# Kernel tuning notes

Measured on AMD Instinct MI355X. Metric: run time of the kernel, lower is better.

## Reference

```python
import jax, jax.numpy as jnp
import numpy as np

H, D = 8, 32          # num_heads, head dim (hidden = 256)
HID = H * D
LRELU = 0.2
NT, NC, E, FIN = 60000, 30000, 200000, 64


def setup_inputs() -> dict:
    key = jax.random.key(0)
    ks = jax.random.split(key, 24)
    s = 0.05
    inp = {
        'x_trans': jax.random.normal(ks[0], (NT, FIN), jnp.float32),
        'x_cc':    jax.random.normal(ks[1], (NC, FIN), jnp.float32),
        'src_c2t': jax.random.randint(ks[2], (E,), 0, NC),
        'dst_c2t': jax.random.randint(ks[3], (E,), 0, NT),
        'src_t2c': jax.random.randint(ks[4], (E,), 0, NT),
        'dst_t2c': jax.random.randint(ks[5], (E,), 0, NC),
        'W_in': jax.random.normal(ks[6], (2, FIN, HID), jnp.float32) * s,
        'b_in': jnp.zeros((2, HID), jnp.float32),
        'Wk': jax.random.normal(ks[7], (2, 2, HID, HID), jnp.float32) * s,
        'bk': jnp.zeros((2, 2, HID), jnp.float32),
        'Wq': jax.random.normal(ks[8], (2, 2, HID, HID), jnp.float32) * s,
        'bq': jnp.zeros((2, 2, HID), jnp.float32),
        'Wv': jax.random.normal(ks[9], (2, 2, HID, HID), jnp.float32) * s,
        'bv': jnp.zeros((2, 2, HID), jnp.float32),
        'Wa': jax.random.normal(ks[10], (2, 2, HID, HID), jnp.float32) * s,
        'ba': jnp.zeros((2, 2, HID), jnp.float32),
        'a_rel': jax.random.normal(ks[11], (2, 2, H, D, D), jnp.float32) * s,
        'm_rel': jax.random.normal(ks[12], (2, 2, H, D, D), jnp.float32) * s,
        'p_rel': jnp.ones((2, 2, H), jnp.float32),
        'skip':  jnp.ones((2, 2), jnp.float32),
        'W_out': jax.random.normal(ks[13], (HID, 64), jnp.float32) * s,
        'b_out': jnp.zeros((64,), jnp.float32),
    }
    return inp


def _hgt_layer(xs, Wk, bk, Wq, bq, Wv, bv, Wa, ba, a_rel, m_rel, p_rel, skip, edges):
    # xs: list of [N_t, HID] per node type; edges: list of (src_type, dst_type, src_idx, dst_idx)
    nt = len(xs)
    k = [(xs[t] @ Wk[t] + bk[t]).reshape(-1, H, D) for t in range(nt)]
    q = [(xs[t] @ Wq[t] + bq[t]).reshape(-1, H, D) for t in range(nt)]
    v = [(xs[t] @ Wv[t] + bv[t]).reshape(-1, H, D) for t in range(nt)]
    agg = [jnp.zeros((xs[t].shape[0], H, D), xs[t].dtype) for t in range(nt)]
    inv_sqrt_d = 1.0 / jnp.sqrt(jnp.float32(D))
    for r, (st, dt, si, di) in enumerate(edges):
        kr = jnp.einsum('nhd,hde->nhe', k[st], a_rel[r])   # relation-transformed keys
        vr = jnp.einsum('nhd,hde->nhe', v[st], m_rel[r])   # relation-transformed messages
        ke, ve, qe = kr[si], vr[si], q[dt][di]             # [E, H, D] gathers
        alpha = jnp.einsum('ehd,ehd->eh', qe, ke) * p_rel[r] * inv_sqrt_d  # [E, H]
        n_dst = xs[dt].shape[0]
        m = jax.ops.segment_max(alpha, di, num_segments=n_dst)
        ex = jnp.exp(alpha - m[di])
        ssum = jax.ops.segment_sum(ex, di, num_segments=n_dst)
        w = ex / (ssum[di] + 1e-16)                         # segment softmax per dst node
        agg[dt] = agg[dt] + jax.ops.segment_sum(ve * w[..., None], di, num_segments=n_dst)
    out = []
    for t in range(nt):
        o = jax.nn.gelu(agg[t].reshape(-1, HID), approximate=False)
        o = o @ Wa[t] + ba[t]
        beta = jax.nn.sigmoid(skip[t])
        out.append(beta * o + (1.0 - beta) * xs[t])
    return out


def reference(x_trans, x_cc, src_c2t, dst_c2t, src_t2c, dst_t2c,
              W_in, b_in, Wk, bk, Wq, bq, Wv, bv, Wa, ba,
              a_rel, m_rel, p_rel, skip, W_out, b_out):
    # per-node-type Linear + in-place relu
    xs = [jax.nn.relu(x_trans @ W_in[0] + b_in[0]),
          jax.nn.relu(x_cc @ W_in[1] + b_in[1])]
    # relation 0: cc_node -> trans_node ; relation 1: trans_node -> cc_node
    edges = [(1, 0, src_c2t, dst_c2t), (0, 1, src_t2c, dst_t2c)]
    n_layers = Wk.shape[0]
    for l in range(n_layers):
        xs = _hgt_layer(xs, Wk[l], bk[l], Wq[l], bq[l], Wv[l], bv[l], Wa[l], ba[l],
                        a_rel[l], m_rel[l], p_rel[l], skip[l], edges)
    # dropout is identity in eval mode
    y = xs[0] @ W_out + b_out
    y = jnp.where(y > 0, y, LRELU * y)                      # LeakyReLU(0.2)
    n = jnp.linalg.norm(y, axis=1, keepdims=True)
    return y / jnp.maximum(n, 1e-12)                        # F.normalize(p=2, dim=1)
```

## Files before the change

kernel.cpp:

```cpp
#include <hip/hip_runtime.h>
#include <hip/hip_bf16.h>
#include <math.h>

#define NTN 60000
#define NCN 30000
#define NED 200000

typedef unsigned short u16;
typedef __attribute__((ext_vector_type(8))) u16 u16x8;
typedef __attribute__((ext_vector_type(8))) __bf16 bf16x8;
typedef __attribute__((ext_vector_type(4))) float f32x4;

static __device__ __forceinline__ float bf2f(u16 u) {
    return __uint_as_float(((unsigned)u) << 16);
}
static __device__ __forceinline__ u16 f2bf(float f) {
    unsigned u = __float_as_uint(f);
    unsigned r = (u + 0x7fffu + ((u >> 16) & 1u)) >> 16;
    return (u16)r;
}

__global__ void fill_u32(unsigned* __restrict__ p, unsigned v, int n) {
    int i = blockIdx.x * blockDim.x + threadIdx.x;
    int stride = gridDim.x * blockDim.x;
    for (; i < n; i += stride) p[i] = v;
}

__global__ void f32_to_bf16(const float* __restrict__ in, u16* __restrict__ out, int n4) {
    int i = blockIdx.x * blockDim.x + threadIdx.x;
    int stride = gridDim.x * blockDim.x;
    for (; i < n4; i += stride) {
        float4 v = ((const float4*)in)[i];
        ushort4 o;
        o.x = f2bf(v.x); o.y = f2bf(v.y); o.z = f2bf(v.z); o.w = f2bf(v.w);
        ((ushort4*)out)[i] = o;
    }
}

__global__ void convTb(const float* __restrict__ in, u16* __restrict__ out,
                       int K, int N, int inStride, int outStride, int nm) {
    int idx = blockIdx.x * blockDim.x + threadIdx.x;
    int per = N * (K >> 2);
    int total = per * nm;
    if (idx >= total) return;
    int mat = idx / per, rem = idx - mat * per;
    int k4 = rem / N, n = rem - k4 * N;
    int k = k4 * 4;
    const float* src = in + (size_t)mat * inStride;
    u16* dst = out + (size_t)mat * outStride;
    ushort4 o;
    o.x = f2bf(src[(size_t)(k + 0) * N + n]);
    o.y = f2bf(src[(size_t)(k + 1) * N + n]);
    o.z = f2bf(src[(size_t)(k + 2) * N + n]);
    o.w = f2bf(src[(size_t)(k + 3) * N + n]);
    *(ushort4*)(dst + (size_t)n * K + k) = o;
}

__global__ void copy_bq(const float* __restrict__ bq, float* __restrict__ bqkv) {
    int lt = blockIdx.x;
    bqkv[lt * 768 + threadIdx.x] = bq[lt * 256 + threadIdx.x];
}

__global__ __launch_bounds__(256) void fuse_weights(
    const float* __restrict__ Wk, const float* __restrict__ bk,
    const float* __restrict__ Wv, const float* __restrict__ bv,
    const float* __restrict__ a_rel, const float* __restrict__ m_rel,
    const float* __restrict__ p_rel,
    float* __restrict__ Wf2, float* __restrict__ bqkv)
{
    __shared__ float kw[256], vw[256];
    const int c = blockIdx.x, lt = blockIdx.y, tid = threadIdx.x;
    const int l = lt >> 1, t = lt & 1;
    const int lr = l * 2 + (t == 1 ? 0 : 1);
    const float* WkP = Wk + (size_t)lt * 65536;
    const float* WvP = Wv + (size_t)lt * 65536;
    const float* ar = a_rel + (size_t)lr * 8192;
    const float* mr = m_rel + (size_t)lr * 8192;
    kw[tid] = WkP[c * 256 + tid];
    vw[tid] = WvP[c * 256 + tid];
    __syncthreads();
    const int h = tid >> 5, e = tid & 31;
    const float s = p_rel[lr * 8 + h] * 0.17677669529663687f;
    float ak = 0.f, av = 0.f;
#pragma unroll 8
    for (int d = 0; d < 32; ++d) {
        ak += kw[h * 32 + d] * ar[h * 1024 + d * 32 + e];
        av += vw[h * 32 + d] * mr[h * 1024 + d * 32 + e];
    }
    float* WkfP = Wf2 + (size_t)lt * 131072;
    WkfP[c * 256 + tid] = ak * s;
    WkfP[65536 + c * 256 + tid] = av;
    if (c == 0) {
        const float* bkP = bk + (size_t)lt * 256;
        const float* bvP = bv + (size_t)lt * 256;
        float bka = 0.f, bva = 0.f;
#pragma unroll 8
        for (int d = 0; d < 32; ++d) {
            bka += bkP[h * 32 + d] * ar[h * 1024 + d * 32 + e];
            bva += bvP[h * 32 + d] * mr[h * 1024 + d * 32 + e];
        }
        bqkv[lt * 768 + 256 + tid] = bka * s;
        bqkv[lt * 768 + 512 + tid] = bva;
    }
}

template <int EPI, int BN, bool OBF>
__global__ __launch_bounds__(256) void gemm_mfma(
    const u16* __restrict__ A, const u16* __restrict__ WT,
    const float* __restrict__ bias, void* __restrict__ Cv,
    int M, int K, int ldC, int NY,
    const u16* __restrict__ xres, const float* __restrict__ skipPtr)
{
    constexpr int ASZ = 64 * 64;
    constexpr int BSZ = BN * 64;
    constexpr int NF = BN / 32;
    __shared__ u16 smem[2 * (ASZ + BSZ)];
    u16* As0 = smem;             u16* Bs0 = smem + ASZ;
    u16* As1 = smem + ASZ + BSZ; u16* Bs1 = As1 + ASZ;

    const int nwg = gridDim.x;
    const int bid = blockIdx.x;
    const int q8 = nwg >> 3, r8 = nwg & 7;
    const int xcd = bid & 7, pos = bid >> 3;
    const int lbid = (xcd < r8) ? xcd * (q8 + 1) + pos
                                : r8 * (q8 + 1) + (xcd - r8) * q8 + pos;
    const int bx = lbid / NY, by = lbid - bx * NY;
    const int m0 = bx * 64, n0 = by * BN;

    const int tid = threadIdx.x;
    const int wave = tid >> 6, lane = tid & 63;
    const int wm = (wave >> 1) * 32, wn = (wave & 1) * (BN / 2);
    f32x4 acc[2][NF];
#pragma unroll
    for (int i = 0; i < 2; ++i)
#pragma unroll
        for (int j = 0; j < NF; ++j) acc[i][j] = (f32x4){0.f, 0.f, 0.f, 0.f};

    const int sr = lane >> 3;
    const int sl = lane & 7;

    auto stage = [&](int k0, u16* Ad, u16* Bd) {
#pragma unroll
        for (int i = 0; i < 2; ++i) {
            int rb = wave * 16 + i * 8;
            int r = rb + sr;
            int gr = m0 + r; gr = gr < M ? gr : M - 1;
            const u16* gp = A + (size_t)gr * K + k0 + ((sl ^ sr) << 3);
            __builtin_amdgcn_global_load_lds(
                (const __attribute__((address_space(1))) void*)gp,
                (__attribute__((address_space(3))) void*)(Ad + rb * 64), 16, 0, 0);
        }
#pragma unroll
        for (int i = 0; i < NF; ++i) {
            int rb = wave * (BN / 4) + i * 8;
            int r = rb + sr;
            const u16* gp = WT + (size_t)(n0 + r) * K + k0 + ((sl ^ sr) << 3);
            __builtin_amdgcn_global_load_lds(
                (const __attribute__((address_space(1))) void*)gp,
                (__attribute__((address_space(3))) void*)(Bd + rb * 64), 16, 0, 0);
        }
    };

    auto compute = [&](const u16* Ab, const u16* Bb) {
#pragma unroll
        for (int kx = 0; kx < 2; ++kx) {
            bf16x8 af[2], bfr[NF];
#pragma unroll
            for (int mf = 0; mf < 2; ++mf) {
                int r = wm + mf * 16 + (lane & 15);
                int slot = (lane >> 4) + kx * 4;
                af[mf] = __builtin_bit_cast(bf16x8,
                    *(const u16x8*)(Ab + r * 64 + ((slot ^ (r & 7)) << 3)));
            }
#pragma unroll
            for (int nf = 0; nf < NF; ++nf) {
                int r = wn + nf * 16 + (lane & 15);
                int slot = (lane >> 4) + kx * 4;
                bfr[nf] = __builtin_bit_cast(bf16x8,
                    *(const u16x8*)(Bb + r * 64 + ((slot ^ (r & 7)) << 3)));
            }
#pragma unroll
            for (int mf = 0; mf < 2; ++mf)
#pragma unroll
                for (int nf = 0; nf < NF; ++nf)
                    acc[mf][nf] = __builtin_amdgcn_mfma_f32_16x16x32_bf16(
                        af[mf], bfr[nf], acc[mf][nf], 0, 0, 0);
        }
    };

    const int nt = K >> 6;
    stage(0, As0, Bs0);
    for (int t = 0; t < nt; ++t) {
        const bool pb = t & 1;
        if (t + 1 < nt) {
            stage((t + 1) << 6, pb ? As0 : As1, pb ? Bs0 : Bs1);
            __builtin_amdgcn_sched_barrier(0);
            if constexpr (BN == 128) asm volatile("s_waitcnt vmcnt(6)" ::: "memory");
            else                     asm volatile("s_waitcnt vmcnt(4)" ::: "memory");
        } else {
            asm volatile("s_waitcnt vmcnt(0)" ::: "memory");
        }
        __builtin_amdgcn_s_barrier();
        __builtin_amdgcn_sched_barrier(0);
        compute(pb ? As1 : As0, pb ? Bs1 : Bs0);
        __builtin_amdgcn_sched_barrier(0);
        __builtin_amdgcn_s_barrier();
        __builtin_amdgcn_sched_barrier(0);
    }

    float beta = 0.f;
    if (EPI == 2) beta = 1.f / (1.f + expf(-skipPtr[0]));

    if constexpr (OBF) {
        constexpr int CLD = BN + 8;
        u16* Ct = smem;
#pragma unroll
        for (int nf = 0; nf < NF; ++nf) {
            int col = wn + nf * 16 + (lane & 15);
            int gcol = n0 + col;
            float bs = bias[gcol];
#pragma unroll
            for (int mf = 0; mf < 2; ++mf) {
#pragma unroll
                for (int j = 0; j < 4; ++j) {
                    int row = wm + mf * 16 + (lane >> 4) * 4 + j;
                    int grow = m0 + row;
                    int gr2 = grow < M ? grow : 0;
                    float c = acc[mf][nf][j] + bs;
                    if (EPI == 1) c = fmaxf(c, 0.f);
                    if (EPI == 2) c = beta * c + (1.f - beta) * bf2f(xres[(size_t)gr2 * ldC + gcol]);
                    if (EPI == 3) c = (c > 0.f) ? c : 0.2f * c;
                    Ct[row * CLD + col] = f2bf(c);
                }
            }
        }
        __syncthreads();
        int row = tid >> 2, c0 = (tid & 3) * (BN / 4);
        int grow = m0 + row;
        if (grow < M) {
            u16* dst = (u16*)Cv + (size_t)grow * ldC + n0 + c0;
            const u16* src = Ct + row * CLD + c0;
#pragma unroll
            for (int i = 0; i < BN / 32; ++i)
                *(u16x8*)(dst + i * 8) = *(const u16x8*)(src + i * 8);
        }
    } else {
#pragma unroll
        for (int nf = 0; nf < NF; ++nf) {
            int gcol = n0 + wn + nf * 16 + (lane & 15);
            float bs = bias[gcol];
#pragma unroll
            for (int mf = 0; mf < 2; ++mf) {
#pragma unroll
                for (int j = 0; j < 4; ++j) {
                    int grow = m0 + wm + mf * 16 + (lane >> 4) * 4 + j;
                    if (grow >= M) continue;
                    float c = acc[mf][nf][j] + bs;
                    if (EPI == 1) c = fmaxf(c, 0.f);
                    if (EPI == 3) c = (c > 0.f) ? c : 0.2f * c;
                    ((float*)Cv)[(size_t)grow * ldC + gcol] = c;
                }
            }
        }
    }
}

__global__ void hist_kernel(const int* __restrict__ di, unsigned* __restrict__ counts, int E) {
    int e = blockIdx.x * blockDim.x + threadIdx.x;
    if (e < E) atomicAdd(&counts[di[e]], 1u);
}

__global__ __launch_bounds__(256) void scan_blocks(
    const unsigned* __restrict__ counts, unsigned* __restrict__ pref,
    unsigned* __restrict__ bsum, int N)
{
    __shared__ unsigned tmp[256];
    int i = blockIdx.x * 256 + threadIdx.x;
    unsigned v = (i < N) ? counts[i] : 0u;
    tmp[threadIdx.x] = v;
    __syncthreads();
    for (int off = 1; off < 256; off <<= 1) {
        unsigned t = (threadIdx.x >= off) ? tmp[threadIdx.x - off] : 0u;
        __syncthreads();
        tmp[threadIdx.x] += t;
        __syncthreads();
    }
    if (i < N) pref[i] = tmp[threadIdx.x] - v;
    if (threadIdx.x == 255) bsum[blockIdx.x] = tmp[255];
}

__global__ __launch_bounds__(256) void scan_top(unsigned* __restrict__ bsum, int NB) {
    __shared__ unsigned tmp[256];
    unsigned v = (threadIdx.x < NB) ? bsum[threadIdx.x] : 0u;
    tmp[threadIdx.x] = v;
    __syncthreads();
    for (int off = 1; off < 256; off <<= 1) {
        unsigned t = (threadIdx.x >= off) ? tmp[threadIdx.x - off] : 0u;
        __syncthreads();
        tmp[threadIdx.x] += t;
        __syncthreads();
    }
    if (threadIdx.x < NB) bsum[threadIdx.x] = tmp[threadIdx.x] - v;
}

__global__ void scan_add(unsigned* __restrict__ pref, const unsigned* __restrict__ bsum,
                         unsigned* __restrict__ cursor, int N) {
    int i = blockIdx.x * 256 + threadIdx.x;
    if (i < N) {
        unsigned s = pref[i] + bsum[blockIdx.x];
        pref[i] = s;
        cursor[i] = s;
    }
}

__global__ void place_kernel(const int* __restrict__ di, const int* __restrict__ si,
                             unsigned* __restrict__ cursor, unsigned* __restrict__ srcout, int E) {
    int e = blockIdx.x * blockDim.x + threadIdx.x;
    if (e < E) {
        unsigned p = atomicAdd(&cursor[di[e]], 1u);
        srcout[p] = (unsigned)si[e];
    }
}

#define TBLK ((NTN + 3) / 4)
__global__ __launch_bounds__(256) void edge_gather2(
    const u16* __restrict__ qkvT, const u16* __restrict__ qkvC,
    const unsigned* __restrict__ rsT, const unsigned* __restrict__ cntT,
    const unsigned* __restrict__ srcT,
    const unsigned* __restrict__ rsC, const unsigned* __restrict__ cntC,
    const unsigned* __restrict__ srcC,
    u16* __restrict__ aggT, u16* __restrict__ aggC)
{
    const int b = blockIdx.x;
    const bool isT = b < TBLK;
    const int n = (isT ? b : b - TBLK) * 4 + (threadIdx.x >> 6);
    const int Ndst = isT ? NTN : NCN;
    if (n >= Ndst) return;
    const u16* qkv_d = isT ? qkvT : qkvC;
    const u16* qkv_s = isT ? qkvC : qkvT;
    const unsigned* rs = isT ? rsT : rsC;
    const unsigned* cnt = isT ? cntT : cntC;
    const unsigned* srcarr = isT ? srcT : srcC;
    u16* agg = isT ? aggT : aggC;

    const int lane = threadIdx.x & 63;
    const int lq = lane & 31;
    const int h = lane >> 5;
    const unsigned start = rs[n], deg = cnt[n];

    if (deg == 0) {
        if (lane < 32)
            *(u16x8*)&agg[(size_t)n * 256 + lq * 8] = (u16x8){0, 0, 0, 0, 0, 0, 0, 0};
        return;
    }

    u16x8 qv = *(const u16x8*)&qkv_d[(size_t)n * 768 + lq * 8];
    float qf[8];
#pragma unroll
    for (int i = 0; i < 8; ++i) qf[i] = bf2f(qv[i]);

    const u16* kvb = qkv_s + 256;
    float m = -INFINITY, s = 0.f;
    float acc[8] = {0.f, 0.f, 0.f, 0.f, 0.f, 0.f, 0.f, 0.f};

    unsigned j = (unsigned)h;
    if (j < deg) {
        unsigned src = srcarr[start + j];
        const u16* rp = kvb + (size_t)src * 768 + lq * 8;
        u16x8 kr = *(const u16x8*)rp;
        u16x8 vr = *(const u16x8*)(rp + 256);
        for (;;) {
            u16x8 kr_n, vr_n;
            const bool more = (j + 2 < deg);
            if (more) {
                unsigned s2 = srcarr[start + j + 2];
                const u16* rp2 = kvb + (size_t)s2 * 768 + lq * 8;
                kr_n = *(const u16x8*)rp2;
                vr_n = *(const u16x8*)(rp2 + 256);
            }
            float kf[8], vf[8];
#pragma unroll
            for (int i = 0; i < 8; ++i) { kf[i] = bf2f(kr[i]); vf[i] = bf2f(vr[i]); }
            float p = qf[0] * kf[0] + qf[1] * kf[1] + qf[2] * kf[2] + qf[3] * kf[3]
                    + qf[4] * kf[4] + qf[5] * kf[5] + qf[6] * kf[6] + qf[7] * kf[7];
            p += __shfl_xor(p, 1);
            p += __shfl_xor(p, 2);
            float mn = fmaxf(m, p);
            float sc = __expf(m - mn);
            float wv = __expf(p - mn);
            s = s * sc + wv;
#pragma unroll
            for (int i = 0; i < 8; ++i) acc[i] = acc[i] * sc + wv * vf[i];
            m = mn;
            if (!more) break;
            kr = kr_n; vr = vr_n; j += 2;
        }
    }

    float mo = __shfl_xor(m, 32);
    float so = __shfl_xor(s, 32);
    float mt = fmaxf(m, mo);
    float sc0 = __expf(m - mt);
    float sco = __expf(mo - mt);
    float st = s * sc0 + so * sco;
    float inv = 1.f / (st + 1e-16f);
    u16x8 ov;
#pragma unroll
    for (int i = 0; i < 8; ++i) {
        float ao = __shfl_xor(acc[i], 32);
        float x = (acc[i] * sc0 + ao * sco) * inv;
        float g = 0.5f * x * (1.f + erff(x * 0.70710678118654752f));
        ov[i] = f2bf(g);
    }
    if (lane < 32)
        *(u16x8*)&agg[(size_t)n * 256 + lq * 8] = ov;
}

__global__ __launch_bounds__(256) void norm_rows(float* __restrict__ y, int M) {
    int row = blockIdx.x * 4 + (threadIdx.x >> 6);
    int lane = threadIdx.x & 63;
    if (row >= M) return;
    float v = y[(size_t)row * 64 + lane];
    float s = v * v;
#pragma unroll
    for (int off = 1; off < 64; off <<= 1) s += __shfl_xor(s, off);
    float n = sqrtf(s);
    y[(size_t)row * 64 + lane] = v / fmaxf(n, 1e-12f);
}

extern "C" void kernel_launch(void* const* d_in, const int* in_sizes, int n_in,
                              void* d_out, int out_size, void* d_ws, size_t ws_size,
                              hipStream_t stream)
{
    const float* x_trans = (const float*)d_in[0];
    const float* x_cc    = (const float*)d_in[1];
    const int* src_c2t   = (const int*)d_in[2];
    const int* dst_c2t   = (const int*)d_in[3];
    const int* src_t2c   = (const int*)d_in[4];
    const int* dst_t2c   = (const int*)d_in[5];
    const float* W_in = (const float*)d_in[6];
    const float* b_in = (const float*)d_in[7];
    const float* Wk   = (const float*)d_in[8];
    const float* bk   = (const float*)d_in[9];
    const float* Wq   = (const float*)d_in[10];
    const float* bq   = (const float*)d_in[11];
    const float* Wv   = (const float*)d_in[12];
    const float* bv   = (const float*)d_in[13];
    const float* Wa   = (const float*)d_in[14];
    const float* ba   = (const float*)d_in[15];
    const float* a_rel = (const float*)d_in[16];
    const float* m_rel = (const float*)d_in[17];
    const float* p_rel = (const float*)d_in[18];
    const float* skip  = (const float*)d_in[19];
    const float* W_out = (const float*)d_in[20];
    const float* b_out = (const float*)d_in[21];

    char* w = (char*)d_ws;
    auto alloc = [&](size_t bytes) { char* p = w; w += (bytes + 255) & ~(size_t)255; return p; };
    u16* xs0  = (u16*)alloc((size_t)NTN * 256 * 2);
    u16* xs1  = (u16*)alloc((size_t)NCN * 256 * 2);
    u16* xin0 = (u16*)alloc((size_t)NTN * 64 * 2);
    u16* xin1 = (u16*)alloc((size_t)NCN * 64 * 2);
    u16* qkv0 = (u16*)alloc((size_t)NTN * 768 * 2);
    u16* qkv1 = (u16*)alloc((size_t)NCN * 768 * 2);
    u16* agg0 = (u16*)alloc((size_t)NTN * 256 * 2);
    u16* agg1 = (u16*)alloc((size_t)NCN * 256 * 2);
    u16* WinT = (u16*)alloc((size_t)2 * 16384 * 2);
    u16* WqkvT= (u16*)alloc((size_t)4 * 196608 * 2);
    u16* WaT  = (u16*)alloc((size_t)4 * 65536 * 2);
    u16* WoutT= (u16*)alloc((size_t)16384 * 2);
    float* Wf2 = (float*)alloc((size_t)4 * 131072 * 4);
    float* bqkv = (float*)alloc((size_t)4 * 768 * 4);
    unsigned* countsT   = (unsigned*)alloc((size_t)NTN * 4);
    unsigned* rowstartT = (unsigned*)alloc((size_t)NTN * 4);
    unsigned* cursorT   = (unsigned*)alloc((size_t)NTN * 4);
    unsigned* srcAT     = (unsigned*)alloc((size_t)NED * 4);
    unsigned* countsC   = (unsigned*)alloc((size_t)NCN * 4);
    unsigned* rowstartC = (unsigned*)alloc((size_t)NCN * 4);
    unsigned* cursorC   = (unsigned*)alloc((size_t)NCN * 4);
    unsigned* srcAC     = (unsigned*)alloc((size_t)NED * 4);
    unsigned* bsum      = (unsigned*)alloc((size_t)256 * 4);
    (void)ws_size; (void)in_sizes; (void)n_in; (void)out_size;

    {
        const int EB = (NED + 255) / 256;
        int NBt = (NTN + 255) / 256;
        fill_u32<<<256, 256, 0, stream>>>(countsT, 0u, NTN);
        hist_kernel<<<EB, 256, 0, stream>>>(dst_c2t, countsT, NED);
        scan_blocks<<<NBt, 256, 0, stream>>>(countsT, rowstartT, bsum, NTN);
        scan_top<<<1, 256, 0, stream>>>(bsum, NBt);
        scan_add<<<NBt, 256, 0, stream>>>(rowstartT, bsum, cursorT, NTN);
        place_kernel<<<EB, 256, 0, stream>>>(dst_c2t, src_c2t, cursorT, srcAT, NED);
        int NBc = (NCN + 255) / 256;
        fill_u32<<<256, 256, 0, stream>>>(countsC, 0u, NCN);
        hist_kernel<<<EB, 256, 0, stream>>>(dst_t2c, countsC, NED);
        scan_blocks<<<NBc, 256, 0, stream>>>(countsC, rowstartC, bsum, NCN);
        scan_top<<<1, 256, 0, stream>>>(bsum, NBc);
        scan_add<<<NBc, 256, 0, stream>>>(rowstartC, bsum, cursorC, NCN);
        place_kernel<<<EB, 256, 0, stream>>>(dst_t2c, src_t2c, cursorC, srcAC, NED);
    }

    fuse_weights<<<dim3(256, 4), 256, 0, stream>>>(Wk, bk, Wv, bv, a_rel, m_rel, p_rel, Wf2, bqkv);
    copy_bq<<<4, 256, 0, stream>>>(bq, bqkv);
    convTb<<<(4 * 16384 + 255) / 256, 256, 0, stream>>>(Wq, WqkvT, 256, 256, 65536, 196608, 4);
    convTb<<<(4 * 16384 + 255) / 256, 256, 0, stream>>>(Wf2, WqkvT + 65536, 256, 256, 131072, 196608, 4);
    convTb<<<(4 * 16384 + 255) / 256, 256, 0, stream>>>(Wf2 + 65536, WqkvT + 131072, 256, 256, 131072, 196608, 4);
    convTb<<<(4 * 16384 + 255) / 256, 256, 0, stream>>>(Wa, WaT, 256, 256, 65536, 65536, 4);
    convTb<<<(2 * 4096 + 255) / 256, 256, 0, stream>>>(W_in, WinT, 64, 256, 16384, 16384, 2);
    convTb<<<(4096 + 255) / 256, 256, 0, stream>>>(W_out, WoutT, 256, 64, 16384, 16384, 1);
    f32_to_bf16<<<1024, 256, 0, stream>>>(x_trans, xin0, NTN * 64 / 4);
    f32_to_bf16<<<1024, 256, 0, stream>>>(x_cc,    xin1, NCN * 64 / 4);

    const int GT = (NTN + 63) / 64, GC = (NCN + 63) / 64;

    gemm_mfma<1, 64, true><<<GT * 4, 256, 0, stream>>>(xin0, WinT, b_in, xs0, NTN, 64, 256, 4, nullptr, nullptr);
    gemm_mfma<1, 64, true><<<GC * 4, 256, 0, stream>>>(xin1, WinT + 16384, b_in + 256, xs1, NCN, 64, 256, 4, nullptr, nullptr);

    for (int l = 0; l < 2; ++l) {
        size_t lt0 = (size_t)(l * 2 + 0), lt1 = (size_t)(l * 2 + 1);

        gemm_mfma<0, 64, true><<<GT * 12, 256, 0, stream>>>(xs0, WqkvT + lt0 * 196608, bqkv + lt0 * 768, qkv0, NTN, 256, 768, 12, nullptr, nullptr);
        gemm_mfma<0, 64, true><<<GC * 12, 256, 0, stream>>>(xs1, WqkvT + lt1 * 196608, bqkv + lt1 * 768, qkv1, NCN, 256, 768, 12, nullptr, nullptr);

        edge_gather2<<<TBLK + (NCN + 3) / 4, 256, 0, stream>>>(
            qkv0, qkv1,
            rowstartT, countsT, srcAT,
            rowstartC, countsC, srcAC,
            agg0, agg1);

        gemm_mfma<2, 64, true><<<GT * 4, 256, 0, stream>>>(agg0, WaT + lt0 * 65536, ba + lt0 * 256, xs0, NTN, 256, 256, 4, xs0, skip + l * 2 + 0);
        gemm_mfma<2, 64, true><<<GC * 4, 256, 0, stream>>>(agg1, WaT + lt1 * 65536, ba + lt1 * 256, xs1, NCN, 256, 256, 4, xs1, skip + l * 2 + 1);
    }

    {
        float* y = (float*)d_out;
        gemm_mfma<3, 64, false><<<GT, 256, 0, stream>>>(xs0, WoutT, b_out, y, NTN, 256, 64, 1, nullptr, nullptr);
        norm_rows<<<NTN / 4, 256, 0, stream>>>(y, NTN);
    }
}
```

Before: 499.3 us.

## Merge per-type GEMM launches and streamline edge gather indexing and softmax

Each pair of per-node-type GEMM launches is merged into one grouped launch that picks operands by block index, which cuts launch count and tail effects. Row start and degree are packed into a single 64-bit entry so the gather does one load instead of two. Source indices are stored pre-multiplied by the row stride, removing a multiply in the hot loop. The online softmax skips the rescale when no lane sees a new maximum, checked with a wave ballot, at the cost of an extra ballot per edge.

Result: faster. 481.7 us (-3.5%).

```diff
diff --git a/kernel.cpp b/kernel.cpp
--- a/kernel.cpp
+++ b/kernel.cpp
@@ -7,6 +7,7 @@
 #define NED 200000
 
 typedef unsigned short u16;
+typedef unsigned long long u64;
 typedef __attribute__((ext_vector_type(8))) u16 u16x8;
 typedef __attribute__((ext_vector_type(8))) __bf16 bf16x8;
 typedef __attribute__((ext_vector_type(4))) float f32x4;
@@ -105,11 +106,15 @@
 }
 
 template <int EPI, int BN, bool OBF>
-__global__ __launch_bounds__(256) void gemm_mfma(
-    const u16* __restrict__ A, const u16* __restrict__ WT,
-    const float* __restrict__ bias, void* __restrict__ Cv,
-    int M, int K, int ldC, int NY,
-    const u16* __restrict__ xres, const float* __restrict__ skipPtr)
+__global__ __launch_bounds__(256) void gemm_mfma2(
+    int nblk0,
+    const u16* __restrict__ A0, const u16* __restrict__ W0, const float* __restrict__ b0,
+    void* __restrict__ C0, int M0, int ldC0, int NY0,
+    const u16* __restrict__ xr0, const float* __restrict__ sk0,
+    const u16* __restrict__ A1, const u16* __restrict__ W1, const float* __restrict__ b1,
+    void* __restrict__ C1, int M1, int ldC1, int NY1,
+    const u16* __restrict__ xr1, const float* __restrict__ sk1,
+    int K)
 {
     constexpr int ASZ = 64 * 64;
     constexpr int BSZ = BN * 64;
@@ -124,7 +129,17 @@
     const int xcd = bid & 7, pos = bid >> 3;
     const int lbid = (xcd < r8) ? xcd * (q8 + 1) + pos
                                 : r8 * (q8 + 1) + (xcd - r8) * q8 + pos;
-    const int bx = lbid / NY, by = lbid - bx * NY;
+
+    const u16* A; const u16* WT; const float* bias; void* Cv;
+    int M, ldC, NY, sb; const u16* xres; const float* skipPtr;
+    if (lbid < nblk0) {
+        A = A0; WT = W0; bias = b0; Cv = C0; M = M0; ldC = ldC0; NY = NY0;
+        xres = xr0; skipPtr = sk0; sb = lbid;
+    } else {
+        A = A1; WT = W1; bias = b1; Cv = C1; M = M1; ldC = ldC1; NY = NY1;
+        xres = xr1; skipPtr = sk1; sb = lbid - nblk0;
+    }
+    const int bx = sb / NY, by = sb - bx * NY;
     const int m0 = bx * 64, n0 = by * BN;
 
     const int tid = threadIdx.x;
@@ -304,12 +319,13 @@
 }
 
 __global__ void scan_add(unsigned* __restrict__ pref, const unsigned* __restrict__ bsum,
-                         unsigned* __restrict__ cursor, int N) {
+                         const unsigned* __restrict__ counts,
+                         unsigned* __restrict__ cursor, u64* __restrict__ rowinfo, int N) {
     int i = blockIdx.x * 256 + threadIdx.x;
     if (i < N) {
         unsigned s = pref[i] + bsum[blockIdx.x];
-        pref[i] = s;
         cursor[i] = s;
+        rowinfo[i] = (u64)s | ((u64)counts[i] << 32);
     }
 }
 
@@ -318,17 +334,15 @@
     int e = blockIdx.x * blockDim.x + threadIdx.x;
     if (e < E) {
         unsigned p = atomicAdd(&cursor[di[e]], 1u);
-        srcout[p] = (unsigned)si[e];
+        srcout[p] = (unsigned)si[e] * 768u;
     }
 }
 
 #define TBLK ((NTN + 3) / 4)
 __global__ __launch_bounds__(256) void edge_gather2(
     const u16* __restrict__ qkvT, const u16* __restrict__ qkvC,
-    const unsigned* __restrict__ rsT, const unsigned* __restrict__ cntT,
-    const unsigned* __restrict__ srcT,
-    const unsigned* __restrict__ rsC, const unsigned* __restrict__ cntC,
-    const unsigned* __restrict__ srcC,
+    const u64* __restrict__ riT, const unsigned* __restrict__ srcT,
+    const u64* __restrict__ riC, const unsigned* __restrict__ srcC,
     u16* __restrict__ aggT, u16* __restrict__ aggC)
 {
     const int b = blockIdx.x;
@@ -338,15 +352,16 @@
     if (n >= Ndst) return;
     const u16* qkv_d = isT ? qkvT : qkvC;
     const u16* qkv_s = isT ? qkvC : qkvT;
-    const unsigned* rs = isT ? rsT : rsC;
-    const unsigned* cnt = isT ? cntT : cntC;
+    const u64* ri = isT ? riT : riC;
     const unsigned* srcarr = isT ? srcT : srcC;
     u16* agg = isT ? aggT : aggC;
 
     const int lane = threadIdx.x & 63;
     const int lq = lane & 31;
     const int h = lane >> 5;
-    const unsigned start = rs[n], deg = cnt[n];
+    const u64 rinfo = ri[n];
+    const unsigned start = (unsigned)rinfo;
+    const unsigned deg = (unsigned)(rinfo >> 32);
 
     if (deg == 0) {
         if (lane < 32)
@@ -359,39 +374,47 @@
 #pragma unroll
     for (int i = 0; i < 8; ++i) qf[i] = bf2f(qv[i]);
 
-    const u16* kvb = qkv_s + 256;
+    const u16* kvb = qkv_s + 256 + lq * 8;
     float m = -INFINITY, s = 0.f;
     float acc[8] = {0.f, 0.f, 0.f, 0.f, 0.f, 0.f, 0.f, 0.f};
 
     unsigned j = (unsigned)h;
     if (j < deg) {
-        unsigned src = srcarr[start + j];
-        const u16* rp = kvb + (size_t)src * 768 + lq * 8;
-        u16x8 kr = *(const u16x8*)rp;
-        u16x8 vr = *(const u16x8*)(rp + 256);
+        unsigned off = srcarr[start + j];
+        u16x8 kr = *(const u16x8*)(kvb + off);
+        u16x8 vr = *(const u16x8*)(kvb + off + 256);
         for (;;) {
             u16x8 kr_n, vr_n;
             const bool more = (j + 2 < deg);
             if (more) {
-                unsigned s2 = srcarr[start + j + 2];
-                const u16* rp2 = kvb + (size_t)s2 * 768 + lq * 8;
-                kr_n = *(const u16x8*)rp2;
-                vr_n = *(const u16x8*)(rp2 + 256);
+                unsigned off2 = srcarr[start + j + 2];
+                kr_n = *(const u16x8*)(kvb + off2);
+                vr_n = *(const u16x8*)(kvb + off2 + 256);
             }
-            float kf[8], vf[8];
-#pragma unroll
-            for (int i = 0; i < 8; ++i) { kf[i] = bf2f(kr[i]); vf[i] = bf2f(vr[i]); }
+            float kf[8];
+#pragma unroll
+            for (int i = 0; i < 8; ++i) kf[i] = bf2f(kr[i]);
             float p = qf[0] * kf[0] + qf[1] * kf[1] + qf[2] * kf[2] + qf[3] * kf[3]
                     + qf[4] * kf[4] + qf[5] * kf[5] + qf[6] * kf[6] + qf[7] * kf[7];
             p += __shfl_xor(p, 1);
             p += __shfl_xor(p, 2);
-            float mn = fmaxf(m, p);
-            float sc = __expf(m - mn);
-            float wv = __expf(p - mn);
-            s = s * sc + wv;
-#pragma unroll
-            for (int i = 0; i < 8; ++i) acc[i] = acc[i] * sc + wv * vf[i];
-            m = mn;
+            float vf[8];
+#pragma unroll
+            for (int i = 0; i < 8; ++i) vf[i] = bf2f(vr[i]);
+            if (__ballot(p > m) == 0ull) {
+                float wv = __expf(p - m);
+                s += wv;
+#pragma unroll
+                for (int i = 0; i < 8; ++i) acc[i] += wv * vf[i];
+            } else {
+                float mn = fmaxf(m, p);
+                float sc = __expf(m - mn);
+                float wv = __expf(p - mn);
+                s = s * sc + wv;
+#pragma unroll
+                for (int i = 0; i < 8; ++i) acc[i] = acc[i] * sc + wv * vf[i];
+                m = mn;
+            }
             if (!more) break;
             kr = kr_n; vr = vr_n; j += 2;
         }
@@ -472,12 +495,14 @@
     float* Wf2 = (float*)alloc((size_t)4 * 131072 * 4);
     float* bqkv = (float*)alloc((size_t)4 * 768 * 4);
     unsigned* countsT   = (unsigned*)alloc((size_t)NTN * 4);
-    unsigned* rowstartT = (unsigned*)alloc((size_t)NTN * 4);
+    unsigned* prefT     = (unsigned*)alloc((size_t)NTN * 4);
     unsigned* cursorT   = (unsigned*)alloc((size_t)NTN * 4);
+    u64* rowinfoT       = (u64*)alloc((size_t)NTN * 8);
     unsigned* srcAT     = (unsigned*)alloc((size_t)NED * 4);
     unsigned* countsC   = (unsigned*)alloc((size_t)NCN * 4);
-    unsigned* rowstartC = (unsigned*)alloc((size_t)NCN * 4);
+    unsigned* prefC     = (unsigned*)alloc((size_t)NCN * 4);
     unsigned* cursorC   = (unsigned*)alloc((size_t)NCN * 4);
+    u64* rowinfoC       = (u64*)alloc((size_t)NCN * 8);
     unsigned* srcAC     = (unsigned*)alloc((size_t)NED * 4);
     unsigned* bsum      = (unsigned*)alloc((size_t)256 * 4);
     (void)ws_size; (void)in_sizes; (void)n_in; (void)out_size;
@@ -487,16 +512,16 @@
         int NBt = (NTN + 255) / 256;
         fill_u32<<<256, 256, 0, stream>>>(countsT, 0u, NTN);
         hist_kernel<<<EB, 256, 0, stream>>>(dst_c2t, countsT, NED);
-        scan_blocks<<<NBt, 256, 0, stream>>>(countsT, rowstartT, bsum, NTN);
+        scan_blocks<<<NBt, 256, 0, stream>>>(countsT, prefT, bsum, NTN);
         scan_top<<<1, 256, 0, stream>>>(bsum, NBt);
-        scan_add<<<NBt, 256, 0, stream>>>(rowstartT, bsum, cursorT, NTN);
+        scan_add<<<NBt, 256, 0, stream>>>(prefT, bsum, countsT, cursorT, rowinfoT, NTN);
         place_kernel<<<EB, 256, 0, stream>>>(dst_c2t, src_c2t, cursorT, srcAT, NED);
         int NBc = (NCN + 255) / 256;
         fill_u32<<<256, 256, 0, stream>>>(countsC, 0u, NCN);
         hist_kernel<<<EB, 256, 0, stream>>>(dst_t2c, countsC, NED);
-        scan_blocks<<<NBc, 256, 0, stream>>>(countsC, rowstartC, bsum, NCN);
+        scan_blocks<<<NBc, 256, 0, stream>>>(countsC, prefC, bsum, NCN);
         scan_top<<<1, 256, 0, stream>>>(bsum, NBc);
-        scan_add<<<NBc, 256, 0, stream>>>(rowstartC, bsum, cursorC, NCN);
+        scan_add<<<NBc, 256, 0, stream>>>(prefC, bsum, countsC, cursorC, rowinfoC, NCN);
         place_kernel<<<EB, 256, 0, stream>>>(dst_t2c, src_t2c, cursorC, srcAC, NED);
     }
 
@@ -513,28 +538,41 @@
 
     const int GT = (NTN + 63) / 64, GC = (NCN + 63) / 64;
 
-    gemm_mfma<1, 64, true><<<GT * 4, 256, 0, stream>>>(xin0, WinT, b_in, xs0, NTN, 64, 256, 4, nullptr, nullptr);
-    gemm_mfma<1, 64, true><<<GC * 4, 256, 0, stream>>>(xin1, WinT + 16384, b_in + 256, xs1, NCN, 64, 256, 4, nullptr, nullptr);
+    gemm_mfma2<1, 64, true><<<GT * 4 + GC * 4, 256, 0, stream>>>(
+        GT * 4,
+        xin0, WinT, b_in, xs0, NTN, 256, 4, nullptr, nullptr,
+        xin1, WinT + 16384, b_in + 256, xs1, NCN, 256, 4, nullptr, nullptr,
+        64);
 
     for (int l = 0; l < 2; ++l) {
         size_t lt0 = (size_t)(l * 2 + 0), lt1 = (size_t)(l * 2 + 1);
 
-        gemm_mfma<0, 64, true><<<GT * 12, 256, 0, stream>>>(xs0, WqkvT + lt0 * 196608, bqkv + lt0 * 768, qkv0, NTN, 256, 768, 12, nullptr, nullptr);
-        gemm_mfma<0, 64, true><<<GC * 12, 256, 0, stream>>>(xs1, WqkvT + lt1 * 196608, bqkv + lt1 * 768, qkv1, NCN, 256, 768, 12, nullptr, nullptr);
+        gemm_mfma2<0, 64, true><<<GT * 12 + GC * 12, 256, 0, stream>>>(
+            GT * 12,
+            xs0, WqkvT + lt0 * 196608, bqkv + lt0 * 768, qkv0, NTN, 768, 12, nullptr, nullptr,
+            xs1, WqkvT + lt1 * 196608, bqkv + lt1 * 768, qkv1, NCN, 768, 12, nullptr, nullptr,
+            256);
 
         edge_gather2<<<TBLK + (NCN + 3) / 4, 256, 0, stream>>>(
             qkv0, qkv1,
-            rowstartT, countsT, srcAT,
-            rowstartC, countsC, srcAC,
+            rowinfoT, srcAT,
+            rowinfoC, srcAC,
             agg0, agg1);
 
-        gemm_mfma<2, 64, true><<<GT * 4, 256, 0, stream>>>(agg0, WaT + lt0 * 65536, ba + lt0 * 256, xs0, NTN, 256, 256, 4, xs0, skip + l * 2 + 0);
-        gemm_mfma<2, 64, true><<<GC * 4, 256, 0, stream>>>(agg1, WaT + lt1 * 65536, ba + lt1 * 256, xs1, NCN, 256, 256, 4, xs1, skip + l * 2 + 1);
+        gemm_mfma2<2, 64, true><<<GT * 4 + GC * 4, 256, 0, stream>>>(
+            GT * 4,
+            agg0, WaT + lt0 * 65536, ba + lt0 * 256, xs0, NTN, 256, 4, xs0, skip + l * 2 + 0,
+            agg1, WaT + lt1 * 65536, ba + lt1 * 256, xs1, NCN, 256, 4, xs1, skip + l * 2 + 1,
+            256);
     }
 
     {
         float* y = (float*)d_out;
-        gemm_mfma<3, 64, false><<<GT, 256, 0, stream>>>(xs0, WoutT, b_out, y, NTN, 256, 64, 1, nullptr, nullptr);
+        gemm_mfma2<3, 64, false><<<GT, 256, 0, stream>>>(
+            GT,
+            xs0, WoutT, b_out, y, NTN, 64, 1, nullptr, nullptr,
+            xs0, WoutT, b_out, y, NTN, 64, 1, nullptr, nullptr,
+            256);
         norm_rows<<<NTN / 4, 256, 0, stream>>>(y, NTN);
     }
 }
```
